# Kernel tuning notes

Measured on AMD Instinct MI355X. Metric: run time of the kernel, lower is better.

The kernel has to match this reference:

```python
import jax, jax.numpy as jnp
import numpy as np

B, S, D, H = 8, 2048, 256, 4
DH = D // H
DFF = 4 * D


def setup_inputs() -> dict:
    key = jax.random.key(0)
    ks = jax.random.split(key, 32)
    w = lambda k, sh: (jax.random.normal(k, sh, jnp.float32) * 0.02)
    inp = {
        'global_feat': jax.random.normal(ks[0], (B, S, D), jnp.float32),
        'local_feat': jax.random.normal(ks[1], (B, S, D), jnp.float32),
        'text_feat': jax.random.normal(ks[2], (B, S, D), jnp.float32),
        'Wl1': w(ks[3], (D, D)), 'bl1': jnp.zeros((D,), jnp.float32),
        'Wl2': w(ks[4], (D, D)), 'bl2': jnp.zeros((D,), jnp.float32),
        'Wg': w(ks[5], (D, D)), 'bg': jnp.zeros((D,), jnp.float32),
        'Wgq': w(ks[6], (D, D)), 'bgq': jnp.zeros((D,), jnp.float32),
        'Wgk': w(ks[7], (D, D)), 'bgk': jnp.zeros((D,), jnp.float32),
        'Wgv': w(ks[8], (D, D)), 'bgv': jnp.zeros((D,), jnp.float32),
        'Wpq': w(ks[9], (D, D)), 'bpq': jnp.zeros((D,), jnp.float32),
        'Wpk': w(ks[10], (D, D)), 'bpk': jnp.zeros((D,), jnp.float32),
        'Wpv': w(ks[11], (D, D)), 'bpv': jnp.zeros((D,), jnp.float32),
        'Wd': w(ks[12], (D, D)), 'bd': jnp.zeros((D,), jnp.float32),
        'Wm1': w(ks[13], (D, DFF)), 'bm1': jnp.zeros((DFF,), jnp.float32),
        'Wm2': w(ks[14], (DFF, D)), 'bm2': jnp.zeros((D,), jnp.float32),
        'Wml': w(ks[15], (D, D)), 'bml': jnp.zeros((D,), jnp.float32),
    }
    return inp


def _heads(x):
    # [B,S,D] -> [B,H,S,DH]
    return x.reshape(B, S, H, DH).transpose(0, 2, 1, 3)


def _merge(x):
    # [B,H,S,DH] -> [B,S,D]
    return x.transpose(0, 2, 1, 3).reshape(B, S, D)


def reference(global_feat, local_feat, text_feat,
              Wl1, bl1, Wl2, bl2, Wg, bg,
              Wgq, bgq, Wgk, bgk, Wgv, bgv,
              Wpq, bpq, Wpk, bpk, Wpv, bpv,
              Wd, bd, Wm1, bm1, Wm2, bm2, Wml, bml):
    scale = 1.0 / jnp.sqrt(jnp.asarray(DH, jnp.float32))
    # embedding projections (dropout inactive in eval mode)
    dup_local = local_feat @ Wl1 + bl1      # local_embedding_1
    local = local_feat @ Wl2 + bl2          # local_embedding_2
    glob = global_feat @ Wg + bg            # global_embedding
    # global branch: Q from global, K/V from local
    gq = _heads(glob @ Wgq + bgq)
    gk = _heads(local @ Wgk + bgk)
    gv = _heads(local @ Wgv + bgv)
    # local branch: Q from duplicate local, K/V from text
    pq = _heads(dup_local @ Wpq + bpq)
    pk = _heads(text_feat @ Wpk + bpk)
    pv = _heads(text_feat @ Wpv + bpv)
    glb_probs = jax.nn.softmax(jnp.einsum('bhqd,bhkd->bhqk', gq, gk) * scale, axis=-1)
    plb_probs = jax.nn.softmax(jnp.einsum('bhqd,bhkd->bhqk', pq, pk) * scale, axis=-1)
    # bridging matmul: fuse probability maps
    plb_enhanced = jnp.einsum('bhqk,bhkl->bhql', glb_probs, plb_probs)
    glb_ctx = _merge(jnp.einsum('bhqk,bhkd->bhqd', glb_probs, gv))
    plb_ctx = _merge(jnp.einsum('bhqk,bhkd->bhqd', plb_enhanced, pv))
    out = (glb_ctx + plb_ctx) @ Wd + bd
    # GPT-style MLP (c_fc -> GELU -> c_proj)
    out = jax.nn.gelu(out @ Wm1 + bm1) @ Wm2 + bm2
    out = out @ Wml + bml
    return out
```

## Files before the change

kernel.cpp:

```cpp
#include <hip/hip_runtime.h>
#include <math.h>

#define Bn 8
#define Sn 2048
#define Dn 256
#define Hn 4
#define DHn 64
#define Mn (Bn*Sn)

typedef short bf16x8 __attribute__((ext_vector_type(8)));
typedef float f32x2  __attribute__((ext_vector_type(2)));
typedef float f32x4  __attribute__((ext_vector_type(4)));
typedef float f32x16 __attribute__((ext_vector_type(16)));
typedef int   i32x4  __attribute__((ext_vector_type(4)));
typedef unsigned short u16;
typedef unsigned int   u32;
typedef unsigned long long u64;

#if defined(__has_builtin)
#if __has_builtin(__builtin_amdgcn_global_load_lds)
#define HAVE_GLL 1
#endif
#if __has_builtin(__builtin_amdgcn_permlane32_swap)
#define HAVE_PLS 1
#endif
#endif
#ifndef HAVE_GLL
#define HAVE_GLL 0
#endif
#ifndef HAVE_PLS
#define HAVE_PLS 0
#endif

__device__ __forceinline__ u16 f2b(float f){
    u32 u = __float_as_uint(f);
    u32 r = (u + 0x7fffu + ((u >> 16) & 1u)) >> 16;
    return (u16)r;
}
__device__ __forceinline__ float b2f(u16 h){ return __uint_as_float(((u32)h) << 16); }
__device__ __forceinline__ u32 cvtpk(float lo, float hi){
    u32 r;
    asm("v_cvt_pk_bf16_f32 %0, %1, %2" : "=v"(r) : "v"(lo), "v"(hi));
    return r;
}

__device__ __forceinline__ float gelu_f(float x){
    const float K1 = 2.3021143113f;
    const float K2 = 0.1029390163f;
    float x2 = x * x;
    float arg = fmaf(x2 * x, K2, x * K1);
    float e = exp2f(arg);
    float r = __builtin_amdgcn_rcpf(e + 1.0f);
    return x - x * r;
}

__device__ __forceinline__ void xcd_map(u32& bx, u32& by, u32& bz){
    const u32 gx = gridDim.x, gy = gridDim.y, gz = gridDim.z;
    if ((gy & 7) == 0){
        const u32 lid = (blockIdx.z * gy + blockIdx.y) * gx + blockIdx.x;
        const u32 xcd = lid & 7;
        u32 c = lid >> 3;
        bx = c % gx;  c /= gx;
        bz = c % gz;  c /= gz;
        by = xcd * (gy >> 3) + c;
    } else {
        bx = blockIdx.x; by = blockIdx.y; bz = blockIdx.z;
    }
}

struct WtArgs {
    const float* src[13];
    int kdim[13], ndim[13], dstoff[13], t0[13], rm[13];
};
struct BcArgs {
    const float* W2[4];
    const float* b1[4];
    const float* b2[4];
    int off[4];
    float* fb;
    int bc0;
};

__global__ __launch_bounds__(256) void prep_k(WtArgs a, u16* __restrict__ dst, BcArgs bc)
{
    __shared__ float tile[32][33];
    int bx = blockIdx.x;
    if (bx >= bc.bc0){
        int p = bx - bc.bc0, aa = threadIdx.x;
        const float* W2 = bc.W2[p];
        const float* b1 = bc.b1[p];
        const float* b2 = bc.b2[p];
        float s = b2[aa];
        for (int j = 0; j < 256; ++j) s = fmaf(b1[j], W2[(size_t)j*256 + aa], s);
        bc.fb[bc.off[p] + aa] = s;
        if (p == 0) bc.fb[1024 + aa] = 0.f;
        return;
    }
    int tb = bx;
    int wi = 0;
    #pragma unroll
    for (int i = 1; i < 13; ++i) if (tb >= a.t0[i]) wi = i;
    int tt = tb - a.t0[wi];
    int N = a.ndim[wi], K = a.kdim[wi];
    int ntn = N >> 5;
    int tn = tt % ntn, tk = tt / ntn;
    int n0 = tn * 32, k0 = tk * 32;
    const float* src = a.src[wi];
    u16* out = dst + a.dstoff[wi];
    int r = threadIdx.x >> 5, c = threadIdx.x & 31;
    if (a.rm[wi]){
        #pragma unroll
        for (int rr = 0; rr < 4; ++rr){
            size_t idx = (size_t)(k0 + r*4 + rr) * N + n0 + c;
            out[idx] = f2b(src[idx]);
        }
        return;
    }
    #pragma unroll
    for (int rr = 0; rr < 4; ++rr)
        tile[r*4+rr][c] = src[(size_t)(k0 + r*4 + rr) * N + n0 + c];
    __syncthreads();
    #pragma unroll
    for (int rr = 0; rr < 4; ++rr)
        out[(size_t)(n0 + r*4 + rr) * K + k0 + c] = f2b(tile[c][r*4+rr]);
}

struct Grp {
    const u16* A[6];
    const u16* Wt[6];
    const float* bias[6];
    void* C[6];
    float scale[6];
};

template<int ACT, int OUTF32>
__global__ __launch_bounds__(256, 4) void gemm_k(Grp g, int N, int K)
{
    u32 bx, by, bz;
    xcd_map(bx, by, bz);

    const u16* __restrict__ A   = g.A[bz];
    const u16* __restrict__ Wt  = g.Wt[bz];
    const float* __restrict__ bias = g.bias[bz];
    void* __restrict__ Cv = g.C[bz];
    const float scale = g.scale[bz];

    __shared__ u16 sm[2][6144];
    const int tid = threadIdx.x;
    const int w = tid >> 6, lane = tid & 63;
    const int l15 = lane & 15, l4 = lane >> 4;
    const int wr = w & 1, wc = w >> 1;
    const int bm = by << 6, bn = bx << 7;
    const int xq = l4 ^ ((lane >> 1) & 3);

    f32x4 acc[4][2];
    #pragma unroll
    for (int nf = 0; nf < 4; ++nf)
        #pragma unroll
        for (int mf = 0; mf < 2; ++mf){
            acc[nf][mf][0]=0.f; acc[nf][mf][1]=0.f; acc[nf][mf][2]=0.f; acc[nf][mf][3]=0.f;
        }

    auto STAGE = [&](int buf, int kt){
        #pragma unroll
        for (int j = 0; j < 3; ++j){
            int ch = w*192 + j*64 + lane;
            int isB = ch >= 256;
            int cc  = isB ? ch - 256 : ch;
            int row = cc >> 2, q = cc & 3;
            int qs  = q ^ ((row >> 1) & 3);
            const u16* src = isB ? (Wt + (size_t)(bn + row) * K + kt + qs*8)
                                 : (A  + (size_t)(bm + row) * K + kt + qs*8);
#if HAVE_GLL
            u16* lb = &sm[buf][(size_t)(w*192 + j*64) * 8];
            __builtin_amdgcn_global_load_lds((const __attribute__((address_space(1))) void*)src,
                                             (__attribute__((address_space(3))) void*)lb, 16, 0, 0);
#else
            *(i32x4*)&sm[buf][(size_t)ch * 8] = *(const i32x4*)src;
#endif
        }
    };

    STAGE(0, 0);
    const int nk = K >> 5;
    for (int t = 0; t < nk; ++t){
        const int cur = t & 1;
        if (t + 1 < nk){
            STAGE(cur ^ 1, (t + 1) << 5);
#if HAVE_GLL
            asm volatile("s_waitcnt vmcnt(3)" ::: "memory");
#endif
        } else {
#if HAVE_GLL
            asm volatile("s_waitcnt vmcnt(0)" ::: "memory");
#endif
        }
        __builtin_amdgcn_s_barrier();
        asm volatile("" ::: "memory");

        const u16* As = sm[cur];
        const u16* Bs = sm[cur] + 2048;
        bf16x8 wf[4], af[2];
        #pragma unroll
        for (int nf = 0; nf < 4; ++nf)
            wf[nf] = *(const bf16x8*)(Bs + (size_t)(wc*64 + nf*16 + l15) * 32 + xq*8);
        #pragma unroll
        for (int mf = 0; mf < 2; ++mf)
            af[mf] = *(const bf16x8*)(As + (size_t)(wr*32 + mf*16 + l15) * 32 + xq*8);
        __builtin_amdgcn_s_setprio(1);
        #pragma unroll
        for (int nf = 0; nf < 4; ++nf)
            #pragma unroll
            for (int mf = 0; mf < 2; ++mf)
                acc[nf][mf] = __builtin_amdgcn_mfma_f32_16x16x32_bf16(wf[nf], af[mf], acc[nf][mf], 0, 0, 0);
        __builtin_amdgcn_s_setprio(0);

        asm volatile("" ::: "memory");
        __builtin_amdgcn_s_barrier();
    }

    #pragma unroll
    for (int nf = 0; nf < 4; ++nf){
        const int n0 = bn + wc*64 + nf*16 + l4*4;
        float4 b4 = *(const float4*)(bias + n0);
        #pragma unroll
        for (int mf = 0; mf < 2; ++mf){
            const int m = bm + wr*32 + mf*16 + l15;
            float r0 = (acc[nf][mf][0] + b4.x) * scale;
            float r1 = (acc[nf][mf][1] + b4.y) * scale;
            float r2 = (acc[nf][mf][2] + b4.z) * scale;
            float r3 = (acc[nf][mf][3] + b4.w) * scale;
            if (ACT){ r0 = gelu_f(r0); r1 = gelu_f(r1); r2 = gelu_f(r2); r3 = gelu_f(r3); }
            if (OUTF32){
                float4 o; o.x = r0; o.y = r1; o.z = r2; o.w = r3;
                *(float4*)((float*)Cv + (size_t)m * N + n0) = o;
            } else {
                u64 p = (u64)cvtpk(r0, r1) | ((u64)cvtpk(r2, r3) << 32);
                *(u64*)((u16*)Cv + (size_t)m * N + n0) = p;
            }
        }
    }
}

struct Grp32 {
    const float* A[6];
    const u16* Wt[6];
    const float* bias[6];
    void* C[6];
    float scale[6];
};

__global__ __launch_bounds__(256, 4) void gemm32_k(Grp32 g, int N, int K)
{
    u32 bx, by, bz;
    xcd_map(bx, by, bz);

    const float* __restrict__ A = g.A[bz];
    const u16* __restrict__ Wt  = g.Wt[bz];
    const float* __restrict__ bias = g.bias[bz];
    void* __restrict__ Cv = g.C[bz];
    const float scale = g.scale[bz];

    __shared__ u16 sm[2][6144];
    const int tid = threadIdx.x;
    const int w = tid >> 6, lane = tid & 63;
    const int l15 = lane & 15, l4 = lane >> 4;
    const int wr = w & 1, wc = w >> 1;
    const int bm = by << 6, bn = bx << 7;
    const int xq = l4 ^ ((lane >> 1) & 3);

    f32x4 acc[4][2];
    #pragma unroll
    for (int nf = 0; nf < 4; ++nf)
        #pragma unroll
        for (int mf = 0; mf < 2; ++mf){
            acc[nf][mf][0]=0.f; acc[nf][mf][1]=0.f; acc[nf][mf][2]=0.f; acc[nf][mf][3]=0.f;
        }

    const int arow = tid >> 2, aq = tid & 3;
    const int aqs = aq ^ ((arow >> 1) & 3);
    const float* Ab = A + (size_t)(bm + arow) * K + aqs*8;
    float4 a0r, a1r;
    auto A_ISSUE = [&](int kt){
        a0r = *(const float4*)(Ab + kt);
        a1r = *(const float4*)(Ab + kt + 4);
    };
    auto A_WRITE = [&](int buf){
        i32x4 o;
        o[0] = (int)cvtpk(a0r.x, a0r.y); o[1] = (int)cvtpk(a0r.z, a0r.w);
        o[2] = (int)cvtpk(a1r.x, a1r.y); o[3] = (int)cvtpk(a1r.z, a1r.w);
        *(i32x4*)&sm[buf][(size_t)tid * 8] = o;
    };
    auto B_STAGE = [&](int buf, int kt){
        #pragma unroll
        for (int j = 0; j < 2; ++j){
            int ch = w*128 + j*64 + lane;
            int row = ch >> 2, q = ch & 3;
            int qs  = q ^ ((row >> 1) & 3);
            const u16* src = Wt + (size_t)(bn + row) * K + kt + qs*8;
#if HAVE_GLL
            u16* lb = &sm[buf][2048 + (size_t)(w*128 + j*64) * 8];
            __builtin_amdgcn_global_load_lds((const __attribute__((address_space(1))) void*)src,
                                             (__attribute__((address_space(3))) void*)lb, 16, 0, 0);
#else
            *(i32x4*)&sm[buf][2048 + (size_t)ch * 8] = *(const i32x4*)src;
#endif
        }
    };

    A_ISSUE(0);
    B_STAGE(0, 0);
    A_WRITE(0);
    __syncthreads();

    const int nk = K >> 5;
    for (int t = 0; t < nk; ++t){
        const int cur = t & 1;
        if (t + 1 < nk){
            A_ISSUE((t + 1) << 5);
            B_STAGE(cur ^ 1, (t + 1) << 5);
#if HAVE_GLL
            asm volatile("s_waitcnt vmcnt(4)" ::: "memory");
#endif
        } else {
#if HAVE_GLL
            asm volatile("s_waitcnt vmcnt(0)" ::: "memory");
#endif
        }
        __builtin_amdgcn_s_barrier();
        asm volatile("" ::: "memory");

        const u16* As = sm[cur];
        const u16* Bs = sm[cur] + 2048;
        bf16x8 wf[4], af[2];
        #pragma unroll
        for (int nf = 0; nf < 4; ++nf)
            wf[nf] = *(const bf16x8*)(Bs + (size_t)(wc*64 + nf*16 + l15) * 32 + xq*8);
        #pragma unroll
        for (int mf = 0; mf < 2; ++mf)
            af[mf] = *(const bf16x8*)(As + (size_t)(wr*32 + mf*16 + l15) * 32 + xq*8);
        __builtin_amdgcn_s_setprio(1);
        #pragma unroll
        for (int nf = 0; nf < 4; ++nf)
            #pragma unroll
            for (int mf = 0; mf < 2; ++mf)
                acc[nf][mf] = __builtin_amdgcn_mfma_f32_16x16x32_bf16(wf[nf], af[mf], acc[nf][mf], 0, 0, 0);
        __builtin_amdgcn_s_setprio(0);

        if (t + 1 < nk) A_WRITE(cur ^ 1);
        asm volatile("" ::: "memory");
        asm volatile("s_waitcnt lgkmcnt(0)" ::: "memory");
        __builtin_amdgcn_s_barrier();
    }

    #pragma unroll
    for (int nf = 0; nf < 4; ++nf){
        const int n0 = bn + wc*64 + nf*16 + l4*4;
        float4 b4 = *(const float4*)(bias + n0);
        #pragma unroll
        for (int mf = 0; mf < 2; ++mf){
            const int m = bm + wr*32 + mf*16 + l15;
            float r0 = (acc[nf][mf][0] + b4.x) * scale;
            float r1 = (acc[nf][mf][1] + b4.y) * scale;
            float r2 = (acc[nf][mf][2] + b4.z) * scale;
            float r3 = (acc[nf][mf][3] + b4.w) * scale;
            u64 p = (u64)cvtpk(r0, r1) | ((u64)cvtpk(r2, r3) << 32);
            *(u64*)((u16*)Cv + (size_t)m * N + n0) = p;
        }
    }
}

template<int FUSE>
__global__ __launch_bounds__(256, 2) void attn_k(const u16* __restrict__ Q, const u16* __restrict__ Kp,
                                                 const u16* __restrict__ Vp, u16* __restrict__ O,
                                                 const u16* __restrict__ ADD)
{
    __shared__ u16 Kl[2][4608];
    __shared__ u16 Vt[2][4608];

    const int tid = threadIdx.x;
    const int w = tid >> 6, lane = tid & 63;
    const int c31 = lane & 31, h = lane >> 5;

    const int lid = blockIdx.x;
    const int nl = (lid & 7) * 64 + (lid >> 3);
    const int bh = nl >> 4;
    const int qb = (nl & 15) << 7;
    const size_t hb = (size_t)(bh >> 2) * Sn * Dn + (size_t)(bh & 3) * DHn;
    const int qrow = qb + w*32 + c31;

    bf16x8 qf[4];
    #pragma unroll
    for (int kc = 0; kc < 4; ++kc)
        qf[kc] = *(const bf16x8*)(Q + hb + (size_t)qrow * Dn + kc*16 + h*8);

    f32x16 ot0, ot1;
    #pragma unroll
    for (int r = 0; r < 16; ++r){ ot0[r] = 0.f; ot1[r] = 0.f; }
    float ll = 0.f;

    int koff0[4], koff1[4];
    #pragma unroll
    for (int kc = 0; kc < 4; ++kc){
        koff0[kc] = c31*72        + kc*16 + h*8;
        koff1[kc] = (32 + c31)*72 + kc*16 + h*8;
    }

    const int krow = tid >> 2, kq = tid & 3;
    const int vk0 = (tid & 15) * 4, vd0 = (tid >> 4) * 4;
    const u32 SEL_LO = 0x05040100u, SEL_HI = 0x07060302u;

    i32x4 krA0, krA1, krB0, krB1;
    u64 vA0, vA1, vA2, vA3, vB0, vB1, vB2, vB3;

    auto LOADA = [&](int kt2){
        const u16* kb = Kp + hb + (size_t)(kt2 + krow) * Dn + kq*8;
        krA0 = *(const i32x4*)kb;
        krA1 = *(const i32x4*)(kb + 32);
        const u16* vb = Vp + hb + (size_t)(kt2 + vk0) * Dn + vd0;
        vA0 = *(const u64*)(vb);
        vA1 = *(const u64*)(vb + Dn);
        vA2 = *(const u64*)(vb + 2*Dn);
        vA3 = *(const u64*)(vb + 3*Dn);
    };
    auto LOADB = [&](int kt2){
        const u16* kb = Kp + hb + (size_t)(kt2 + krow) * Dn + kq*8;
        krB0 = *(const i32x4*)kb;
        krB1 = *(const i32x4*)(kb + 32);
        const u16* vb = Vp + hb + (size_t)(kt2 + vk0) * Dn + vd0;
        vB0 = *(const u64*)(vb);
        vB1 = *(const u64*)(vb + Dn);
        vB2 = *(const u64*)(vb + 2*Dn);
        vB3 = *(const u64*)(vb + 3*Dn);
    };
    auto WRITEA = [&](int buf){
        *(i32x4*)&Kl[buf][(size_t)krow*72 + kq*8]      = krA0;
        *(i32x4*)&Kl[buf][(size_t)krow*72 + kq*8 + 32] = krA1;
        u32 a0 = (u32)vA0, a1 = (u32)vA1, a2 = (u32)vA2, a3 = (u32)vA3;
        u32 b0 = (u32)(vA0 >> 32), b1 = (u32)(vA1 >> 32), b2 = (u32)(vA2 >> 32), b3 = (u32)(vA3 >> 32);
        u64 wd0 = (u64)__builtin_amdgcn_perm(a1, a0, SEL_LO) | ((u64)__builtin_amdgcn_perm(a3, a2, SEL_LO) << 32);
        u64 wd1 = (u64)__builtin_amdgcn_perm(a1, a0, SEL_HI) | ((u64)__builtin_amdgcn_perm(a3, a2, SEL_HI) << 32);
        u64 wd2 = (u64)__builtin_amdgcn_perm(b1, b0, SEL_LO) | ((u64)__builtin_amdgcn_perm(b3, b2, SEL_LO) << 32);
        u64 wd3 = (u64)__builtin_amdgcn_perm(b1, b0, SEL_HI) | ((u64)__builtin_amdgcn_perm(b3, b2, SEL_HI) << 32);
        *(u64*)&Vt[buf][(size_t)(vd0 + 0)*72 + vk0] = wd0;
        *(u64*)&Vt[buf][(size_t)(vd0 + 1)*72 + vk0] = wd1;
        *(u64*)&Vt[buf][(size_t)(vd0 + 2)*72 + vk0] = wd2;
        *(u64*)&Vt[buf][(size_t)(vd0 + 3)*72 + vk0] = wd3;
    };
    auto WRITEB = [&](int buf){
        *(i32x4*)&Kl[buf][(size_t)krow*72 + kq*8]      = krB0;
        *(i32x4*)&Kl[buf][(size_t)krow*72 + kq*8 + 32] = krB1;
        u32 a0 = (u32)vB0, a1 = (u32)vB1, a2 = (u32)vB2, a3 = (u32)vB3;
        u32 b0 = (u32)(vB0 >> 32), b1 = (u32)(vB1 >> 32), b2 = (u32)(vB2 >> 32), b3 = (u32)(vB3 >> 32);
        u64 wd0 = (u64)__builtin_amdgcn_perm(a1, a0, SEL_LO) | ((u64)__builtin_amdgcn_perm(a3, a2, SEL_LO) << 32);
        u64 wd1 = (u64)__builtin_amdgcn_perm(a1, a0, SEL_HI) | ((u64)__builtin_amdgcn_perm(a3, a2, SEL_HI) << 32);
        u64 wd2 = (u64)__builtin_amdgcn_perm(b1, b0, SEL_LO) | ((u64)__builtin_amdgcn_perm(b3, b2, SEL_LO) << 32);
        u64 wd3 = (u64)__builtin_amdgcn_perm(b1, b0, SEL_HI) | ((u64)__builtin_amdgcn_perm(b3, b2, SEL_HI) << 32);
        *(u64*)&Vt[buf][(size_t)(vd0 + 0)*72 + vk0] = wd0;
        *(u64*)&Vt[buf][(size_t)(vd0 + 1)*72 + vk0] = wd1;
        *(u64*)&Vt[buf][(size_t)(vd0 + 2)*72 + vk0] = wd2;
        *(u64*)&Vt[buf][(size_t)(vd0 + 3)*72 + vk0] = wd3;
    };

    auto COMPUTE = [&](int c){
        f32x16 s0, s1;
        #pragma unroll
        for (int r = 0; r < 16; ++r){ s0[r] = 0.f; s1[r] = 0.f; }
        __builtin_amdgcn_s_setprio(1);
        #pragma unroll
        for (int kc = 0; kc < 4; ++kc){
            bf16x8 k0 = *(const bf16x8*)&Kl[c][koff0[kc]];
            bf16x8 k1 = *(const bf16x8*)&Kl[c][koff1[kc]];
            s0 = __builtin_amdgcn_mfma_f32_32x32x16_bf16(k0, qf[kc], s0, 0, 0, 0);
            s1 = __builtin_amdgcn_mfma_f32_32x32x16_bf16(k1, qf[kc], s1, 0, 0, 0);
        }
        __builtin_amdgcn_s_setprio(0);

        f32x2 pp0[8], pp1[8];
        f32x2 rv = {0.f, 0.f};
        #pragma unroll
        for (int r = 0; r < 8; ++r){
            pp0[r][0] = exp2f(s0[2*r]); pp0[r][1] = exp2f(s0[2*r+1]);
            pp1[r][0] = exp2f(s1[2*r]); pp1[r][1] = exp2f(s1[2*r+1]);
            rv += pp0[r];
            rv += pp1[r];
        }
        ll += rv[0] + rv[1];

        __builtin_amdgcn_s_setprio(1);
        #pragma unroll
        for (int kc = 0; kc < 4; ++kc){
            const int iA = 2*kc, iB = 2*kc + 1;
            u32 wA0, wA1, wB0, wB1;
            if (kc < 2){
                wA0 = cvtpk(pp0[iA*2+0][0], pp0[iA*2+0][1]);
                wA1 = cvtpk(pp0[iA*2+1][0], pp0[iA*2+1][1]);
                wB0 = cvtpk(pp0[iB*2+0][0], pp0[iB*2+0][1]);
                wB1 = cvtpk(pp0[iB*2+1][0], pp0[iB*2+1][1]);
            } else {
                wA0 = cvtpk(pp1[(iA-4)*2+0][0], pp1[(iA-4)*2+0][1]);
                wA1 = cvtpk(pp1[(iA-4)*2+1][0], pp1[(iA-4)*2+1][1]);
                wB0 = cvtpk(pp1[(iB-4)*2+0][0], pp1[(iB-4)*2+0][1]);
                wB1 = cvtpk(pp1[(iB-4)*2+1][0], pp1[(iB-4)*2+1][1]);
            }
            i32x4 pw;
#if HAVE_PLS
            {
                auto r02 = __builtin_amdgcn_permlane32_swap((int)wA0, (int)wB0, false, false);
                auto r13 = __builtin_amdgcn_permlane32_swap((int)wA1, (int)wB1, false, false);
                pw[0] = r02[0]; pw[1] = r13[0]; pw[2] = r02[1]; pw[3] = r13[1];
            }
#else
            {
                u32 s0v = h ? wA0 : wB0, s1v = h ? wA1 : wB1;
                u32 g0 = (u32)__shfl_xor((int)s0v, 32);
                u32 g1 = (u32)__shfl_xor((int)s1v, 32);
                pw[0] = (int)(h ? g0 : wA0);
                pw[1] = (int)(h ? g1 : wA1);
                pw[2] = (int)(h ? wB0 : g0);
                pw[3] = (int)(h ? wB1 : g1);
            }
#endif
            bf16x8 pb = *(bf16x8*)&pw;
            bf16x8 va  = *(const bf16x8*)&Vt[c][koff0[kc]];
            bf16x8 vb2 = *(const bf16x8*)&Vt[c][koff1[kc]];
            ot0 = __builtin_amdgcn_mfma_f32_32x32x16_bf16(va,  pb, ot0, 0, 0, 0);
            ot1 = __builtin_amdgcn_mfma_f32_32x32x16_bf16(vb2, pb, ot1, 0, 0, 0);
        }
        __builtin_amdgcn_s_setprio(0);
    };

    LOADA(0);
    WRITEA(0);
    LOADB(1 << 6);
    asm volatile("s_waitcnt lgkmcnt(0)" ::: "memory");
    __builtin_amdgcn_s_barrier();
    asm volatile("" ::: "memory");

    for (int tp = 0; tp < 16; ++tp){
        if (tp < 15) LOADA((2*tp + 2) << 6);
        COMPUTE(0);
        WRITEB(1);
        asm volatile("s_waitcnt lgkmcnt(0)" ::: "memory");
        __builtin_amdgcn_s_barrier();
        asm volatile("" ::: "memory");

        if (tp < 15) LOADB((2*tp + 3) << 6);
        COMPUTE(1);
        if (tp < 15) WRITEA(0);
        asm volatile("s_waitcnt lgkmcnt(0)" ::: "memory");
        __builtin_amdgcn_s_barrier();
        asm volatile("" ::: "memory");
    }

    ll += __shfl_xor(ll, 32);
    float inv = 1.0f / ll;
    #pragma unroll
    for (int rg = 0; rg < 4; ++rg){
        int d0 = 8*rg + 4*h;
        float r0 = ot0[4*rg+0]*inv, r1 = ot0[4*rg+1]*inv, r2 = ot0[4*rg+2]*inv, r3 = ot0[4*rg+3]*inv;
        float x0 = ot1[4*rg+0]*inv, x1 = ot1[4*rg+1]*inv, x2 = ot1[4*rg+2]*inv, x3 = ot1[4*rg+3]*inv;
        if (FUSE){
            u64 ga = *(const u64*)&ADD[hb + (size_t)qrow * Dn + d0];
            u64 gb = *(const u64*)&ADD[hb + (size_t)qrow * Dn + 32 + d0];
            r0 += b2f((u16)ga);         r1 += b2f((u16)(ga >> 16));
            r2 += b2f((u16)(ga >> 32)); r3 += b2f((u16)(ga >> 48));
            x0 += b2f((u16)gb);         x1 += b2f((u16)(gb >> 16));
            x2 += b2f((u16)(gb >> 32)); x3 += b2f((u16)(gb >> 48));
        }
        *(u64*)&O[hb + (size_t)qrow * Dn + d0]      = (u64)cvtpk(r0, r1) | ((u64)cvtpk(r2, r3) << 32);
        *(u64*)&O[hb + (size_t)qrow * Dn + 32 + d0] = (u64)cvtpk(x0, x1) | ((u64)cvtpk(x2, x3) << 32);
    }
}

extern "C" void kernel_launch(void* const* d_in, const int* in_sizes, int n_in,
                              void* d_out, int out_size, void* d_ws, size_t ws_size,
                              hipStream_t stream)
{
    (void)in_sizes; (void)n_in; (void)out_size; (void)ws_size;

    const float* gf  = (const float*)d_in[0];
    const float* lf  = (const float*)d_in[1];
    const float* tf  = (const float*)d_in[2];
    const float* Wl1 = (const float*)d_in[3];  const float* bl1 = (const float*)d_in[4];
    const float* Wl2 = (const float*)d_in[5];  const float* bl2 = (const float*)d_in[6];
    const float* Wg  = (const float*)d_in[7];  const float* bg  = (const float*)d_in[8];
    const float* Wgq = (const float*)d_in[9];  const float* bgq = (const float*)d_in[10];
    const float* Wgk = (const float*)d_in[11]; const float* bgk = (const float*)d_in[12];
    const float* Wgv = (const float*)d_in[13]; const float* bgv = (const float*)d_in[14];
    const float* Wpq = (const float*)d_in[15]; const float* bpq = (const float*)d_in[16];
    const float* bpk = (const float*)d_in[18];
    const float* bpv = (const float*)d_in[20];
    const float* bd  = (const float*)d_in[22];
    const float* bm1 = (const float*)d_in[24];
    const float* bm2 = (const float*)d_in[26];
    const float* Wml = (const float*)d_in[27]; const float* bml = (const float*)d_in[28];

    const float C1 = 0.18033688011112042f;

    u16* ws = (u16*)d_ws;
    const size_t U = (size_t)Mn * Dn;
    u16* S[9];
    for (int i = 0; i < 9; ++i) S[i] = ws + (size_t)i * U;
    u16* wtb = ws + 9 * U;

    const int sq = 65536;
    u16* Wpqt = wtb + 0*sq;  u16* Wgqt = wtb + 1*sq;  u16* Wgkt = wtb + 2*sq;  u16* Wgvt = wtb + 3*sq;
    u16* Wpkt = wtb + 4*sq;  u16* Wpvt = wtb + 5*sq;  u16* Wdt  = wtb + 6*sq;  u16* Wmlt = wtb + 7*sq;
    u16* Wm1t  = wtb + 524288;
    u16* Wm2t  = wtb + 786432;
    u16* Wl1rm = wtb + 1048576;
    u16* Wl2rm = wtb + 1114112;
    u16* Wgrm  = wtb + 1179648;
    u16* Wcpqt = wtb + 1245184;
    u16* Wcgqt = wtb + 1310720;
    u16* Wcgkt = wtb + 1376256;
    u16* Wcgvt = wtb + 1441792;
    float* fb  = (float*)(wtb + 1507328);

    WtArgs wa;
    const float* wsrc[13] = {Wpq, Wgq, Wgk, Wgv, (const float*)d_in[17], (const float*)d_in[19],
                             (const float*)d_in[21], Wml,
                             (const float*)d_in[23], (const float*)d_in[25], Wl1, Wl2, Wg};
    const int wdst[13] = {0, sq, 2*sq, 3*sq, 4*sq, 5*sq, 6*sq, 7*sq, 524288, 786432,
                          1048576, 1114112, 1179648};
    for (int i = 0; i < 13; ++i){
        wa.src[i] = wsrc[i];
        wa.kdim[i] = 256; wa.ndim[i] = 256;
        wa.dstoff[i] = wdst[i];
        wa.rm[i] = (i >= 10);
    }
    wa.ndim[8] = 1024;
    wa.kdim[9] = 1024;
    int acc_t = 0;
    for (int i = 0; i < 13; ++i){
        wa.t0[i] = acc_t;
        acc_t += (wa.ndim[i] >> 5) * (wa.kdim[i] >> 5);
    }
    BcArgs bc;
    bc.W2[0] = Wpq; bc.W2[1] = Wgq; bc.W2[2] = Wgk; bc.W2[3] = Wgv;
    bc.b1[0] = bl1; bc.b1[1] = bg;  bc.b1[2] = bl2; bc.b1[3] = bl2;
    bc.b2[0] = bpq; bc.b2[1] = bgq; bc.b2[2] = bgk; bc.b2[3] = bgv;
    bc.off[0] = 0; bc.off[1] = 256; bc.off[2] = 512; bc.off[3] = 768;
    bc.fb = fb; bc.bc0 = acc_t;
    prep_k<<<dim3(acc_t + 4), 256, 0, stream>>>(wa, wtb, bc);

    auto GN = [&](const Grp& g, int ng, int M, int N, int K, int act, int of32){
        dim3 gr(N / 128, M / 64, ng);
        if (act)        gemm_k<1,0><<<gr, 256, 0, stream>>>(g, N, K);
        else if (of32)  gemm_k<0,1><<<gr, 256, 0, stream>>>(g, N, K);
        else            gemm_k<0,0><<<gr, 256, 0, stream>>>(g, N, K);
    };
    auto G1 = [&](const u16* A, const u16* Wt_, const float* b, void* C, int M, int N, int K,
                  float sc, int act, int of32){
        Grp g{};
        g.A[0] = A; g.Wt[0] = Wt_; g.bias[0] = b; g.C[0] = C; g.scale[0] = sc;
        GN(g, 1, M, N, K, act, of32);
    };

    {
        Grp g{};
        g.A[0] = Wpqt; g.Wt[0] = Wl1rm; g.bias[0] = fb + 1024; g.C[0] = Wcpqt; g.scale[0] = 1.f;
        g.A[1] = Wgqt; g.Wt[1] = Wgrm;  g.bias[1] = fb + 1024; g.C[1] = Wcgqt; g.scale[1] = 1.f;
        g.A[2] = Wgkt; g.Wt[2] = Wl2rm; g.bias[2] = fb + 1024; g.C[2] = Wcgkt; g.scale[2] = 1.f;
        g.A[3] = Wgvt; g.Wt[3] = Wl2rm; g.bias[3] = fb + 1024; g.C[3] = Wcgvt; g.scale[3] = 1.f;
        GN(g, 4, 256, 256, 256, 0, 0);
    }

    {
        Grp32 g{};
        g.A[0] = lf; g.Wt[0] = Wcpqt; g.bias[0] = fb + 0;   g.C[0] = S[3]; g.scale[0] = C1;
        g.A[1] = gf; g.Wt[1] = Wcgqt; g.bias[1] = fb + 256; g.C[1] = S[6]; g.scale[1] = C1;
        g.A[2] = lf; g.Wt[2] = Wcgkt; g.bias[2] = fb + 512; g.C[2] = S[7]; g.scale[2] = 1.f;
        g.A[3] = lf; g.Wt[3] = Wcgvt; g.bias[3] = fb + 768; g.C[3] = S[8]; g.scale[3] = 1.f;
        g.A[4] = tf; g.Wt[4] = Wpkt;  g.bias[4] = bpk;      g.C[4] = S[4]; g.scale[4] = 1.f;
        g.A[5] = tf; g.Wt[5] = Wpvt;  g.bias[5] = bpv;      g.C[5] = S[5]; g.scale[5] = 1.f;
        dim3 gr(2, Mn / 64, 6);
        gemm32_k<<<gr, 256, 0, stream>>>(g, 256, 256);
    }

    attn_k<1><<<dim3(512), 256, 0, stream>>>(S[3], S[4], S[5], S[0], S[8]);
    attn_k<0><<<dim3(512), 256, 0, stream>>>(S[6], S[7], S[0], S[1], nullptr);

    G1(S[1], Wdt,  bd,  S[2],  Mn, 256,  256,  1.f, 0, 0);
    G1(S[2], Wm1t, bm1, S[3],  Mn, 1024, 256,  1.f, 1, 0);
    G1(S[3], Wm2t, bm2, S[7],  Mn, 256,  1024, 1.f, 0, 0);
    G1(S[7], Wmlt, bml, d_out, Mn, 256,  256,  1.f, 0, 1);
}
```

Measured before the change: 217.8 us.

## Concatenate projection weights to share fp32 input reads across Q/K/V GEMMs

Merges the six separate fp32-input projection GEMMs into three wide GEMMs (local→[pq|gk|gv] N=768, text→[pk|pv] N=512, global→gq N=256). Each fp32 activation is then read once instead of up to three times, and the attention kernels take per-tensor row strides so they can read the interleaved outputs directly. The grid now launches blocks that exit early for narrower groups, and the attention loads become strided with larger row pitches.

```diff
diff --git a/kernel.cpp b/kernel.cpp
--- a/kernel.cpp
+++ b/kernel.cpp
@@ -73,10 +73,10 @@
     int kdim[13], ndim[13], dstoff[13], t0[13], rm[13];
 };
 struct BcArgs {
-    const float* W2[4];
-    const float* b1[4];
-    const float* b2[4];
-    int off[4];
+    const float* W2[6];
+    const float* b1[6];
+    const float* b2[6];
+    int off[6];
     float* fb;
     int bc0;
 };
@@ -87,11 +87,13 @@
     int bx = blockIdx.x;
     if (bx >= bc.bc0){
         int p = bx - bc.bc0, aa = threadIdx.x;
-        const float* W2 = bc.W2[p];
-        const float* b1 = bc.b1[p];
         const float* b2 = bc.b2[p];
         float s = b2[aa];
-        for (int j = 0; j < 256; ++j) s = fmaf(b1[j], W2[(size_t)j*256 + aa], s);
+        if (bc.b1[p]){
+            const float* W2 = bc.W2[p];
+            const float* b1 = bc.b1[p];
+            for (int j = 0; j < 256; ++j) s = fmaf(b1[j], W2[(size_t)j*256 + aa], s);
+        }
         bc.fb[bc.off[p] + aa] = s;
         if (p == 0) bc.fb[1024 + aa] = 0.f;
         return;
@@ -126,11 +128,11 @@
 }
 
 struct Grp {
-    const u16* A[6];
-    const u16* Wt[6];
-    const float* bias[6];
-    void* C[6];
-    float scale[6];
+    const u16* A[4];
+    const u16* Wt[4];
+    const float* bias[4];
+    void* C[4];
+    float scale[4];
 };
 
 template<int ACT, int OUTF32>
@@ -243,23 +245,29 @@
 }
 
 struct Grp32 {
-    const float* A[6];
-    const u16* Wt[6];
-    const float* bias[6];
-    void* C[6];
-    float scale[6];
+    const float* A[3];
+    const u16* Wt[3];
+    const float* bias[3];
+    void* C[3];
+    float scale[3];
+    int N[3];
+    int c1lim[3];
 };
 
-__global__ __launch_bounds__(256, 4) void gemm32_k(Grp32 g, int N, int K)
+__global__ __launch_bounds__(256, 4) void gemm32_k(Grp32 g, int K)
 {
     u32 bx, by, bz;
     xcd_map(bx, by, bz);
+
+    const int N = g.N[bz];
+    if ((int)(bx << 7) >= N) return;
 
     const float* __restrict__ A = g.A[bz];
     const u16* __restrict__ Wt  = g.Wt[bz];
     const float* __restrict__ bias = g.bias[bz];
     void* __restrict__ Cv = g.C[bz];
     const float scale = g.scale[bz];
+    const int c1lim = g.c1lim[bz];
 
     __shared__ u16 sm[2][6144];
     const int tid = threadIdx.x;
@@ -357,13 +365,14 @@
     for (int nf = 0; nf < 4; ++nf){
         const int n0 = bn + wc*64 + nf*16 + l4*4;
         float4 b4 = *(const float4*)(bias + n0);
+        const float sc = (n0 < c1lim) ? scale : 1.0f;
         #pragma unroll
         for (int mf = 0; mf < 2; ++mf){
             const int m = bm + wr*32 + mf*16 + l15;
-            float r0 = (acc[nf][mf][0] + b4.x) * scale;
-            float r1 = (acc[nf][mf][1] + b4.y) * scale;
-            float r2 = (acc[nf][mf][2] + b4.z) * scale;
-            float r3 = (acc[nf][mf][3] + b4.w) * scale;
+            float r0 = (acc[nf][mf][0] + b4.x) * sc;
+            float r1 = (acc[nf][mf][1] + b4.y) * sc;
+            float r2 = (acc[nf][mf][2] + b4.z) * sc;
+            float r3 = (acc[nf][mf][3] + b4.w) * sc;
             u64 p = (u64)cvtpk(r0, r1) | ((u64)cvtpk(r2, r3) << 32);
             *(u64*)((u16*)Cv + (size_t)m * N + n0) = p;
         }
@@ -373,7 +382,8 @@
 template<int FUSE>
 __global__ __launch_bounds__(256, 2) void attn_k(const u16* __restrict__ Q, const u16* __restrict__ Kp,
                                                  const u16* __restrict__ Vp, u16* __restrict__ O,
-                                                 const u16* __restrict__ ADD)
+                                                 const u16* __restrict__ ADD,
+                                                 int qs, int ks, int vs, int os, int as_)
 {
     __shared__ u16 Kl[2][4608];
     __shared__ u16 Vt[2][4608];
@@ -386,13 +396,18 @@
     const int nl = (lid & 7) * 64 + (lid >> 3);
     const int bh = nl >> 4;
     const int qb = (nl & 15) << 7;
-    const size_t hb = (size_t)(bh >> 2) * Sn * Dn + (size_t)(bh & 3) * DHn;
+    const int bb = bh >> 2, hh2 = bh & 3;
+    const size_t bQ = (size_t)bb * Sn * qs + (size_t)hh2 * DHn;
+    const size_t bK = (size_t)bb * Sn * ks + (size_t)hh2 * DHn;
+    const size_t bV = (size_t)bb * Sn * vs + (size_t)hh2 * DHn;
+    const size_t bO = (size_t)bb * Sn * os + (size_t)hh2 * DHn;
+    const size_t bA = (size_t)bb * Sn * as_ + (size_t)hh2 * DHn;
     const int qrow = qb + w*32 + c31;
 
     bf16x8 qf[4];
     #pragma unroll
     for (int kc = 0; kc < 4; ++kc)
-        qf[kc] = *(const bf16x8*)(Q + hb + (size_t)qrow * Dn + kc*16 + h*8);
+        qf[kc] = *(const bf16x8*)(Q + bQ + (size_t)qrow * qs + kc*16 + h*8);
 
     f32x16 ot0, ot1;
     #pragma unroll
@@ -414,24 +429,24 @@
     u64 vA0, vA1, vA2, vA3, vB0, vB1, vB2, vB3;
 
     auto LOADA = [&](int kt2){
-        const u16* kb = Kp + hb + (size_t)(kt2 + krow) * Dn + kq*8;
+        const u16* kb = Kp + bK + (size_t)(kt2 + krow) * ks + kq*8;
         krA0 = *(const i32x4*)kb;
         krA1 = *(const i32x4*)(kb + 32);
-        const u16* vb = Vp + hb + (size_t)(kt2 + vk0) * Dn + vd0;
+        const u16* vb = Vp + bV + (size_t)(kt2 + vk0) * vs + vd0;
         vA0 = *(const u64*)(vb);
-        vA1 = *(const u64*)(vb + Dn);
-        vA2 = *(const u64*)(vb + 2*Dn);
-        vA3 = *(const u64*)(vb + 3*Dn);
+        vA1 = *(const u64*)(vb + vs);
+        vA2 = *(const u64*)(vb + 2*vs);
+        vA3 = *(const u64*)(vb + 3*vs);
     };
     auto LOADB = [&](int kt2){
-        const u16* kb = Kp + hb + (size_t)(kt2 + krow) * Dn + kq*8;
+        const u16* kb = Kp + bK + (size_t)(kt2 + krow) * ks + kq*8;
         krB0 = *(const i32x4*)kb;
         krB1 = *(const i32x4*)(kb + 32);
-        const u16* vb = Vp + hb + (size_t)(kt2 + vk0) * Dn + vd0;
+        const u16* vb = Vp + bV + (size_t)(kt2 + vk0) * vs + vd0;
         vB0 = *(const u64*)(vb);
-        vB1 = *(const u64*)(vb + Dn);
-        vB2 = *(const u64*)(vb + 2*Dn);
-        vB3 = *(const u64*)(vb + 3*Dn);
+        vB1 = *(const u64*)(vb + vs);
+        vB2 = *(const u64*)(vb + 2*vs);
+        vB3 = *(const u64*)(vb + 3*vs);
     };
     auto WRITEA = [&](int buf){
         *(i32x4*)&Kl[buf][(size_t)krow*72 + kq*8]      = krA0;
@@ -561,15 +576,15 @@
         float r0 = ot0[4*rg+0]*inv, r1 = ot0[4*rg+1]*inv, r2 = ot0[4*rg+2]*inv, r3 = ot0[4*rg+3]*inv;
         float x0 = ot1[4*rg+0]*inv, x1 = ot1[4*rg+1]*inv, x2 = ot1[4*rg+2]*inv, x3 = ot1[4*rg+3]*inv;
         if (FUSE){
-            u64 ga = *(const u64*)&ADD[hb + (size_t)qrow * Dn + d0];
-            u64 gb = *(const u64*)&ADD[hb + (size_t)qrow * Dn + 32 + d0];
+            u64 ga = *(const u64*)&ADD[bA + (size_t)qrow * as_ + d0];
+            u64 gb = *(const u64*)&ADD[bA + (size_t)qrow * as_ + 32 + d0];
             r0 += b2f((u16)ga);         r1 += b2f((u16)(ga >> 16));
             r2 += b2f((u16)(ga >> 32)); r3 += b2f((u16)(ga >> 48));
             x0 += b2f((u16)gb);         x1 += b2f((u16)(gb >> 16));
             x2 += b2f((u16)(gb >> 32)); x3 += b2f((u16)(gb >> 48));
         }
-        *(u64*)&O[hb + (size_t)qrow * Dn + d0]      = (u64)cvtpk(r0, r1) | ((u64)cvtpk(r2, r3) << 32);
-        *(u64*)&O[hb + (size_t)qrow * Dn + 32 + d0] = (u64)cvtpk(x0, x1) | ((u64)cvtpk(x2, x3) << 32);
+        *(u64*)&O[bO + (size_t)qrow * os + d0]      = (u64)cvtpk(r0, r1) | ((u64)cvtpk(r2, r3) << 32);
+        *(u64*)&O[bO + (size_t)qrow * os + 32 + d0] = (u64)cvtpk(x0, x1) | ((u64)cvtpk(x2, x3) << 32);
     }
 }
 
@@ -604,18 +619,20 @@
     for (int i = 0; i < 9; ++i) S[i] = ws + (size_t)i * U;
     u16* wtb = ws + 9 * U;
 
+    u16* Slf = S[3];
+    u16* Stf = S[6];
+    u16* Sgq = S[8];
+
     const int sq = 65536;
     u16* Wpqt = wtb + 0*sq;  u16* Wgqt = wtb + 1*sq;  u16* Wgkt = wtb + 2*sq;  u16* Wgvt = wtb + 3*sq;
-    u16* Wpkt = wtb + 4*sq;  u16* Wpvt = wtb + 5*sq;  u16* Wdt  = wtb + 6*sq;  u16* Wmlt = wtb + 7*sq;
+    u16* Wpkt = wtb + 4*sq;
+    u16* Wdt  = wtb + 6*sq;  u16* Wmlt = wtb + 7*sq;
     u16* Wm1t  = wtb + 524288;
     u16* Wm2t  = wtb + 786432;
     u16* Wl1rm = wtb + 1048576;
     u16* Wl2rm = wtb + 1114112;
     u16* Wgrm  = wtb + 1179648;
-    u16* Wcpqt = wtb + 1245184;
-    u16* Wcgqt = wtb + 1310720;
-    u16* Wcgkt = wtb + 1376256;
-    u16* Wcgvt = wtb + 1441792;
+    u16* WC0   = wtb + 1245184;
     float* fb  = (float*)(wtb + 1507328);
 
     WtArgs wa;
@@ -638,12 +655,12 @@
         acc_t += (wa.ndim[i] >> 5) * (wa.kdim[i] >> 5);
     }
     BcArgs bc;
-    bc.W2[0] = Wpq; bc.W2[1] = Wgq; bc.W2[2] = Wgk; bc.W2[3] = Wgv;
-    bc.b1[0] = bl1; bc.b1[1] = bg;  bc.b1[2] = bl2; bc.b1[3] = bl2;
-    bc.b2[0] = bpq; bc.b2[1] = bgq; bc.b2[2] = bgk; bc.b2[3] = bgv;
-    bc.off[0] = 0; bc.off[1] = 256; bc.off[2] = 512; bc.off[3] = 768;
+    bc.W2[0] = Wpq; bc.W2[1] = Wgk; bc.W2[2] = Wgv; bc.W2[3] = Wgq; bc.W2[4] = nullptr; bc.W2[5] = nullptr;
+    bc.b1[0] = bl1; bc.b1[1] = bl2; bc.b1[2] = bl2; bc.b1[3] = bg;  bc.b1[4] = nullptr; bc.b1[5] = nullptr;
+    bc.b2[0] = bpq; bc.b2[1] = bgk; bc.b2[2] = bgv; bc.b2[3] = bgq; bc.b2[4] = bpk;     bc.b2[5] = bpv;
+    bc.off[0] = 0; bc.off[1] = 256; bc.off[2] = 512; bc.off[3] = 768; bc.off[4] = 1280; bc.off[5] = 1536;
     bc.fb = fb; bc.bc0 = acc_t;
-    prep_k<<<dim3(acc_t + 4), 256, 0, stream>>>(wa, wtb, bc);
+    prep_k<<<dim3(acc_t + 6), 256, 0, stream>>>(wa, wtb, bc);
 
     auto GN = [&](const Grp& g, int ng, int M, int N, int K, int act, int of32){
         dim3 gr(N / 128, M / 64, ng);
@@ -660,27 +677,26 @@
 
     {
         Grp g{};
-        g.A[0] = Wpqt; g.Wt[0] = Wl1rm; g.bias[0] = fb + 1024; g.C[0] = Wcpqt; g.scale[0] = 1.f;
-        g.A[1] = Wgqt; g.Wt[1] = Wgrm;  g.bias[1] = fb + 1024; g.C[1] = Wcgqt; g.scale[1] = 1.f;
-        g.A[2] = Wgkt; g.Wt[2] = Wl2rm; g.bias[2] = fb + 1024; g.C[2] = Wcgkt; g.scale[2] = 1.f;
-        g.A[3] = Wgvt; g.Wt[3] = Wl2rm; g.bias[3] = fb + 1024; g.C[3] = Wcgvt; g.scale[3] = 1.f;
+        g.A[0] = Wpqt; g.Wt[0] = Wl1rm; g.bias[0] = fb + 1024; g.C[0] = WC0;          g.scale[0] = 1.f;
+        g.A[1] = Wgkt; g.Wt[1] = Wl2rm; g.bias[1] = fb + 1024; g.C[1] = WC0 + sq;     g.scale[1] = 1.f;
+        g.A[2] = Wgvt; g.Wt[2] = Wl2rm; g.bias[2] = fb + 1024; g.C[2] = WC0 + 2*sq;   g.scale[2] = 1.f;
+        g.A[3] = Wgqt; g.Wt[3] = Wgrm;  g.bias[3] = fb + 1024; g.C[3] = WC0 + 3*sq;   g.scale[3] = 1.f;
         GN(g, 4, 256, 256, 256, 0, 0);
     }
 
     {
         Grp32 g{};
-        g.A[0] = lf; g.Wt[0] = Wcpqt; g.bias[0] = fb + 0;   g.C[0] = S[3]; g.scale[0] = C1;
-        g.A[1] = gf; g.Wt[1] = Wcgqt; g.bias[1] = fb + 256; g.C[1] = S[6]; g.scale[1] = C1;
-        g.A[2] = lf; g.Wt[2] = Wcgkt; g.bias[2] = fb + 512; g.C[2] = S[7]; g.scale[2] = 1.f;
-        g.A[3] = lf; g.Wt[3] = Wcgvt; g.bias[3] = fb + 768; g.C[3] = S[8]; g.scale[3] = 1.f;
-        g.A[4] = tf; g.Wt[4] = Wpkt;  g.bias[4] = bpk;      g.C[4] = S[4]; g.scale[4] = 1.f;
-        g.A[5] = tf; g.Wt[5] = Wpvt;  g.bias[5] = bpv;      g.C[5] = S[5]; g.scale[5] = 1.f;
-        dim3 gr(2, Mn / 64, 6);
-        gemm32_k<<<gr, 256, 0, stream>>>(g, 256, 256);
-    }
-
-    attn_k<1><<<dim3(512), 256, 0, stream>>>(S[3], S[4], S[5], S[0], S[8]);
-    attn_k<0><<<dim3(512), 256, 0, stream>>>(S[6], S[7], S[0], S[1], nullptr);
+        g.A[0] = lf; g.Wt[0] = WC0;        g.bias[0] = fb;        g.C[0] = Slf; g.scale[0] = C1;  g.N[0] = 768; g.c1lim[0] = 256;
+        g.A[1] = tf; g.Wt[1] = Wpkt;       g.bias[1] = fb + 1280; g.C[1] = Stf; g.scale[1] = 1.f; g.N[1] = 512; g.c1lim[1] = 0;
+        g.A[2] = gf; g.Wt[2] = WC0 + 3*sq; g.bias[2] = fb + 768;  g.C[2] = Sgq; g.scale[2] = C1;  g.N[2] = 256; g.c1lim[2] = 256;
+        dim3 gr(6, Mn / 64, 3);
+        gemm32_k<<<gr, 256, 0, stream>>>(g, 256);
+    }
+
+    attn_k<1><<<dim3(512), 256, 0, stream>>>(Slf, Stf, Stf + 256, S[0], Slf + 512,
+                                             768, 512, 512, 256, 768);
+    attn_k<0><<<dim3(512), 256, 0, stream>>>(Sgq, Slf + 256, S[0], S[1], nullptr,
+                                             256, 768, 256, 256, 0);
 
     G1(S[1], Wdt,  bd,  S[2],  Mn, 256,  256,  1.f, 0, 0);
     G1(S[2], Wm1t, bm1, S[3],  Mn, 1024, 256,  1.f, 1, 0);
```

Result: slower. 222.3 us (+2.1%).

## Split attention over key halves with fp32 partials and separate reduce kernel

Applied to the files above, without the earlier changes.

Each attention launch is split into two blocks per query tile, each covering half of the key sequence. The grid doubles to 1024 blocks and launch bounds rise to 4 blocks per CU, to raise parallelism and occupancy. Unnormalized fp32 outputs and row sums go to a workspace buffer, and a new reduce kernel combines them, normalizes, applies the optional residual add and converts to bf16. In exchange it adds sizeable fp32 partial write and read traffic plus two extra launches, and it relies on the existing softmax not tracking a running max so the halves can be summed directly.

```diff
diff --git a/kernel.cpp b/kernel.cpp
--- a/kernel.cpp
+++ b/kernel.cpp
@@ -370,10 +370,9 @@
     }
 }
 
-template<int FUSE>
-__global__ __launch_bounds__(256, 2) void attn_k(const u16* __restrict__ Q, const u16* __restrict__ Kp,
-                                                 const u16* __restrict__ Vp, u16* __restrict__ O,
-                                                 const u16* __restrict__ ADD)
+__global__ __launch_bounds__(256, 4) void attn_part_k(const u16* __restrict__ Q, const u16* __restrict__ Kp,
+                                                      const u16* __restrict__ Vp, float* __restrict__ Op,
+                                                      float* __restrict__ llb)
 {
     __shared__ u16 Kl[2][4608];
     __shared__ u16 Vt[2][4608];
@@ -383,11 +382,15 @@
     const int c31 = lane & 31, h = lane >> 5;
 
     const int lid = blockIdx.x;
-    const int nl = (lid & 7) * 64 + (lid >> 3);
-    const int bh = nl >> 4;
-    const int qb = (nl & 15) << 7;
-    const size_t hb = (size_t)(bh >> 2) * Sn * Dn + (size_t)(bh & 3) * DHn;
+    const int nl = (lid & 7) * 128 + (lid >> 3);
+    const int half = nl & 1;
+    const int rst = nl >> 1;
+    const int bh = rst >> 4;
+    const int qb = (rst & 15) << 7;
+    const int bb = bh >> 2, hh2 = bh & 3;
+    const size_t hb = (size_t)bb * Sn * Dn + (size_t)hh2 * DHn;
     const int qrow = qb + w*32 + c31;
+    const int kt0 = half << 10;
 
     bf16x8 qf[4];
     #pragma unroll
@@ -530,47 +533,71 @@
         __builtin_amdgcn_s_setprio(0);
     };
 
-    LOADA(0);
+    LOADA(kt0);
     WRITEA(0);
-    LOADB(1 << 6);
+    LOADB(kt0 + 64);
     asm volatile("s_waitcnt lgkmcnt(0)" ::: "memory");
     __builtin_amdgcn_s_barrier();
     asm volatile("" ::: "memory");
 
-    for (int tp = 0; tp < 16; ++tp){
-        if (tp < 15) LOADA((2*tp + 2) << 6);
+    for (int tp = 0; tp < 8; ++tp){
+        if (tp < 7) LOADA(kt0 + ((2*tp + 2) << 6));
         COMPUTE(0);
         WRITEB(1);
         asm volatile("s_waitcnt lgkmcnt(0)" ::: "memory");
         __builtin_amdgcn_s_barrier();
         asm volatile("" ::: "memory");
 
-        if (tp < 15) LOADB((2*tp + 3) << 6);
+        if (tp < 7) LOADB(kt0 + ((2*tp + 3) << 6));
         COMPUTE(1);
-        if (tp < 15) WRITEA(0);
+        if (tp < 7) WRITEA(0);
         asm volatile("s_waitcnt lgkmcnt(0)" ::: "memory");
         __builtin_amdgcn_s_barrier();
         asm volatile("" ::: "memory");
     }
 
     ll += __shfl_xor(ll, 32);
-    float inv = 1.0f / ll;
+    const size_t U4 = (size_t)Mn * 256;
+    float* op = Op + (size_t)half * U4 + ((size_t)bb * Sn + qrow) * 256 + hh2 * DHn;
     #pragma unroll
     for (int rg = 0; rg < 4; ++rg){
         int d0 = 8*rg + 4*h;
-        float r0 = ot0[4*rg+0]*inv, r1 = ot0[4*rg+1]*inv, r2 = ot0[4*rg+2]*inv, r3 = ot0[4*rg+3]*inv;
-        float x0 = ot1[4*rg+0]*inv, x1 = ot1[4*rg+1]*inv, x2 = ot1[4*rg+2]*inv, x3 = ot1[4*rg+3]*inv;
-        if (FUSE){
-            u64 ga = *(const u64*)&ADD[hb + (size_t)qrow * Dn + d0];
-            u64 gb = *(const u64*)&ADD[hb + (size_t)qrow * Dn + 32 + d0];
-            r0 += b2f((u16)ga);         r1 += b2f((u16)(ga >> 16));
-            r2 += b2f((u16)(ga >> 32)); r3 += b2f((u16)(ga >> 48));
-            x0 += b2f((u16)gb);         x1 += b2f((u16)(gb >> 16));
-            x2 += b2f((u16)(gb >> 32)); x3 += b2f((u16)(gb >> 48));
-        }
-        *(u64*)&O[hb + (size_t)qrow * Dn + d0]      = (u64)cvtpk(r0, r1) | ((u64)cvtpk(r2, r3) << 32);
-        *(u64*)&O[hb + (size_t)qrow * Dn + 32 + d0] = (u64)cvtpk(x0, x1) | ((u64)cvtpk(x2, x3) << 32);
-    }
+        float4 v0; v0.x = ot0[4*rg+0]; v0.y = ot0[4*rg+1]; v0.z = ot0[4*rg+2]; v0.w = ot0[4*rg+3];
+        float4 v1; v1.x = ot1[4*rg+0]; v1.y = ot1[4*rg+1]; v1.z = ot1[4*rg+2]; v1.w = ot1[4*rg+3];
+        *(float4*)(op + d0)      = v0;
+        *(float4*)(op + 32 + d0) = v1;
+    }
+    if (h == 0)
+        llb[(size_t)half * (Mn * Hn) + (size_t)bh * Sn + qrow] = ll;
+}
+
+template<int FUSE>
+__global__ __launch_bounds__(256) void reduce_k(const float* __restrict__ Op, const float* __restrict__ llb,
+                                                u16* __restrict__ O, const u16* __restrict__ ADD)
+{
+    const size_t U4 = (size_t)Mn * 256;
+    int idx = blockIdx.x * 256 + threadIdx.x;
+    int row = idx >> 6;
+    int c4  = (idx & 63) << 2;
+    int head = c4 >> 6;
+    int s = row & (Sn - 1);
+    int b = row >> 11;
+    size_t lli = (size_t)(b * Hn + head) * Sn + s;
+    float la = llb[lli];
+    float lb = llb[(size_t)(Mn * Hn) + lli];
+    float inv = 1.0f / (la + lb);
+    float4 va = *(const float4*)(Op + (size_t)row * 256 + c4);
+    float4 vb = *(const float4*)(Op + U4 + (size_t)row * 256 + c4);
+    float r0 = (va.x + vb.x) * inv;
+    float r1 = (va.y + vb.y) * inv;
+    float r2 = (va.z + vb.z) * inv;
+    float r3 = (va.w + vb.w) * inv;
+    if (FUSE){
+        u64 ga = *(const u64*)&ADD[(size_t)row * 256 + c4];
+        r0 += b2f((u16)ga);         r1 += b2f((u16)(ga >> 16));
+        r2 += b2f((u16)(ga >> 32)); r3 += b2f((u16)(ga >> 48));
+    }
+    *(u64*)&O[(size_t)row * 256 + c4] = (u64)cvtpk(r0, r1) | ((u64)cvtpk(r2, r3) << 32);
 }
 
 extern "C" void kernel_launch(void* const* d_in, const int* in_sizes, int n_in,
@@ -617,6 +644,8 @@
     u16* Wcgkt = wtb + 1376256;
     u16* Wcgvt = wtb + 1441792;
     float* fb  = (float*)(wtb + 1507328);
+    float* Op  = (float*)(wtb + 1572864);
+    float* llb = Op + 2 * (size_t)Mn * 256;
 
     WtArgs wa;
     const float* wsrc[13] = {Wpq, Wgq, Wgk, Wgv, (const float*)d_in[17], (const float*)d_in[19],
@@ -679,8 +708,10 @@
         gemm32_k<<<gr, 256, 0, stream>>>(g, 256, 256);
     }
 
-    attn_k<1><<<dim3(512), 256, 0, stream>>>(S[3], S[4], S[5], S[0], S[8]);
-    attn_k<0><<<dim3(512), 256, 0, stream>>>(S[6], S[7], S[0], S[1], nullptr);
+    attn_part_k<<<dim3(1024), 256, 0, stream>>>(S[3], S[4], S[5], Op, llb);
+    reduce_k<1><<<dim3(Mn / 4), 256, 0, stream>>>(Op, llb, S[0], S[8]);
+    attn_part_k<<<dim3(1024), 256, 0, stream>>>(S[6], S[7], S[0], Op, llb);
+    reduce_k<0><<<dim3(Mn / 4), 256, 0, stream>>>(Op, llb, S[1], nullptr);
 
     G1(S[1], Wdt,  bd,  S[2],  Mn, 256,  256,  1.f, 0, 0);
     G1(S[2], Wm1t, bm1, S[3],  Mn, 1024, 256,  1.f, 1, 0);
```

After: 355.1 us. 63.1% more time.
